# Performance work log

Hardware: AMD Instinct MI355X
Metric: run time of the kernel (lower is better)

## Reference

```python
import jax, jax.numpy as jnp
import numpy as np

N_FEAT = 512
K = 4
H = 128
N_PAIRS = N_FEAT * (N_FEAT - 1) // 2  # 130816

# Upper-triangle pair indices in the same (j1, j2>j1) row-major order as the loops
_I1, _I2 = np.triu_indices(N_FEAT, k=1)
_I1 = jnp.asarray(_I1)
_I2 = jnp.asarray(_I2)


def setup_inputs() -> dict:
    key = jax.random.key(0)
    ks = jax.random.split(key, 8)
    B = 512
    x = jax.random.normal(ks[0], (B, N_FEAT), dtype=jnp.float32)
    fm_w = jax.random.normal(ks[1], (N_FEAT, K), dtype=jnp.float32) * 0.05
    w1 = jax.random.normal(ks[2], (N_FEAT, H), dtype=jnp.float32) * (1.0 / np.sqrt(N_FEAT))
    b1 = jnp.zeros((H,), dtype=jnp.float32)
    w2 = jax.random.normal(ks[3], (H, H), dtype=jnp.float32) * (1.0 / np.sqrt(H))
    b2 = jnp.zeros((H,), dtype=jnp.float32)
    wo = jax.random.normal(ks[4], (N_PAIRS + H, 1), dtype=jnp.float32) * 0.001
    bo = jnp.zeros((1,), dtype=jnp.float32)
    return {"x": x, "fm_w": fm_w, "w1": w1, "b1": b1, "w2": w2, "b2": b2, "wo": wo, "bo": bo}


def reference(x, fm_w, w1, b1, w2, b2, wo, bo):
    # FM pairwise interactions: <w_j1, w_j2> * x[:, j1] * x[:, j2] for j1 < j2.
    # The original unrolls O(B * n^2) tiny 1xK matmuls; algebraically this is a
    # gather of the Gram matrix S = W W^T at the upper-triangle pairs.
    S = fm_w @ fm_w.T                      # [n, n], tiny (512x512)
    pair_dot = S[_I1, _I2]                 # [n_pairs]
    fm = x[:, _I1] * x[:, _I2] * pair_dot  # [B, n_pairs] -- dominant memory traffic

    # Deep part: two relu Dense layers
    h1 = jax.nn.relu(x @ w1 + b1)          # [B, 128]
    h2 = jax.nn.relu(h1 @ w2 + b2)         # [B, 128]

    feat = jnp.concatenate([fm, h2], axis=1)  # [B, n_pairs + 128]
    out = jax.nn.sigmoid(feat @ wo + bo)       # [B, 1]
    return out
```

## Files before the change

### kernel.cpp

```cpp
#include <hip/hip_runtime.h>
#include <math.h>

#define NF 512
#define HD 128
#define NB 512
#define NPAIRS 130816

#define WS_ACC 262144

__device__ __forceinline__ int xswz(int j, int h) {
  int a = (j << 5) + (h << 4);
  a ^= (j & 0x60);
  a ^= ((j & 0x80) >> 3);
  return a >> 2;
}

__global__ __launch_bounds__(256) void k_build(
    const float* __restrict__ fmw, const float* __restrict__ wo,
    float* __restrict__ ws) {
  if (blockIdx.x == 1024) {
    int t = threadIdx.x;
    ws[WS_ACC + t] = 0.f;
    ws[WS_ACC + 256 + t] = 0.f;
    return;
  }
  int t = blockIdx.x * 256 + threadIdx.x;
  int j1 = t >> 9, j2 = t & 511;
  const float4* fw = (const float4*)fmw;
  float4 a = fw[j1], b = fw[j2];
  float dot = a.x * b.x + a.y * b.y + a.z * b.z + a.w * b.w;
  float m = 0.f;
  if (j2 > j1) {
    int idx = j1 * (1023 - j1) / 2 + (j2 - j1 - 1);
    m = dot * wo[idx];
  }
  ws[t] = m;
}

__global__ __launch_bounds__(256, 2) void k_fm(
    const float* __restrict__ x, float* __restrict__ ws) {
  __shared__ float xt[4096];
  __shared__ float red[4][8];
  const int tid = threadIdx.x;
  const int bg = blockIdx.x >> 3;
  const int jc = blockIdx.x & 7;
  const int b0 = bg * 8;

  #pragma unroll
  for (int half = 0; half < 2; ++half) {
    int j = tid + half * 256;
    float xr[8];
    #pragma unroll
    for (int r = 0; r < 8; ++r) xr[r] = x[(b0 + r) * NF + j];
    *(float4*)&xt[xswz(j, 0)] = make_float4(xr[0], xr[1], xr[2], xr[3]);
    *(float4*)&xt[xswz(j, 1)] = make_float4(xr[4], xr[5], xr[6], xr[7]);
  }
  __syncthreads();

  const int j1g = tid & 7;
  const int j2s = tid >> 3;
  const int j1base = jc * 64 + j1g * 8;
  const int j2base = j2s * 16;

  float tmp[8][8];
  #pragma unroll
  for (int i = 0; i < 8; ++i)
    #pragma unroll
    for (int r = 0; r < 8; ++r) tmp[i][r] = 0.f;

  #pragma unroll
  for (int c = 0; c < 4; ++c) {
    float xv[4][8];
    #pragma unroll
    for (int e = 0; e < 4; ++e) {
      int j2 = j2base + c * 4 + e;
      float4 lo = *(const float4*)&xt[xswz(j2, 0)];
      float4 hi = *(const float4*)&xt[xswz(j2, 1)];
      xv[e][0] = lo.x; xv[e][1] = lo.y; xv[e][2] = lo.z; xv[e][3] = lo.w;
      xv[e][4] = hi.x; xv[e][5] = hi.y; xv[e][6] = hi.z; xv[e][7] = hi.w;
    }
    #pragma unroll
    for (int i = 0; i < 8; ++i) {
      const float4 m4 = *(const float4*)&ws[(j1base + i) * NF + j2base + c * 4];
      float mm[4] = {m4.x, m4.y, m4.z, m4.w};
      #pragma unroll
      for (int e = 0; e < 4; ++e)
        #pragma unroll
        for (int r = 0; r < 8; ++r)
          tmp[i][r] += mm[e] * xv[e][r];
    }
  }

  float acc[8];
  #pragma unroll
  for (int r = 0; r < 8; ++r) acc[r] = 0.f;
  #pragma unroll
  for (int i = 0; i < 8; ++i) {
    int j1 = j1base + i;
    float4 lo = *(const float4*)&xt[xswz(j1, 0)];
    float4 hi = *(const float4*)&xt[xswz(j1, 1)];
    float xj[8] = {lo.x, lo.y, lo.z, lo.w, hi.x, hi.y, hi.z, hi.w};
    #pragma unroll
    for (int r = 0; r < 8; ++r) acc[r] += tmp[i][r] * xj[r];
  }

  #pragma unroll
  for (int off = 32; off > 0; off >>= 1)
    #pragma unroll
    for (int r = 0; r < 8; ++r) acc[r] += __shfl_down(acc[r], off, 64);
  const int wave = tid >> 6, lane = tid & 63;
  if (lane == 0)
    #pragma unroll
    for (int r = 0; r < 8; ++r) red[wave][r] = acc[r];
  __syncthreads();
  if (tid < 8) {
    float s = red[0][tid] + red[1][tid] + red[2][tid] + red[3][tid];
    atomicAdd(&ws[WS_ACC + b0 + tid], s);
  }
}

__global__ __launch_bounds__(256) void k_deep(
    const float* __restrict__ x, const float* __restrict__ w1,
    const float* __restrict__ b1, const float* __restrict__ w2,
    const float* __restrict__ b2v, const float* __restrict__ wo,
    const float* __restrict__ bo, const float* __restrict__ ws,
    float* __restrict__ out) {
  __shared__ float xs[2][512];
  __shared__ float p1[2][2][128];
  __shared__ float h1[2][128];
  __shared__ float p2[2][2][128];
  __shared__ float wpart[4];
  const int tid = threadIdx.x;
  const int b0 = blockIdx.x * 2;
  const int h = tid & 127, jh = tid >> 7;

  #pragma unroll
  for (int r = 0; r < 2; ++r) {
    xs[r][tid] = x[(b0 + r) * NF + tid];
    xs[r][tid + 256] = x[(b0 + r) * NF + tid + 256];
  }
  __syncthreads();

  float a0 = 0.f, a1 = 0.f;
  const float* w1p = w1 + h;
  for (int j = 0; j < 256; ++j) {
    int jj = jh * 256 + j;
    float w = w1p[jj * 128];
    a0 += xs[0][jj] * w;
    a1 += xs[1][jj] * w;
  }
  p1[jh][0][h] = a0;
  p1[jh][1][h] = a1;
  __syncthreads();
  {
    int r = jh;
    float v = p1[0][r][h] + p1[1][r][h] + b1[h];
    h1[r][h] = v > 0.f ? v : 0.f;
  }
  __syncthreads();

  float c0 = 0.f, c1 = 0.f;
  const float* w2p = w2 + h;
  for (int k = 0; k < 64; ++k) {
    int kk = jh * 64 + k;
    float w = w2p[kk * 128];
    c0 += h1[0][kk] * w;
    c1 += h1[1][kk] * w;
  }
  p2[jh][0][h] = c0;
  p2[jh][1][h] = c1;
  __syncthreads();

  float val;
  {
    int r = jh;
    float v = p2[0][r][h] + p2[1][r][h] + b2v[h];
    v = v > 0.f ? v : 0.f;
    val = v * wo[NPAIRS + h];
  }
  #pragma unroll
  for (int off = 32; off > 0; off >>= 1) val += __shfl_down(val, off, 64);
  const int wave = tid >> 6, lane = tid & 63;
  if (lane == 0) wpart[wave] = val;
  __syncthreads();
  if (tid < 2) {
    float z = wpart[tid * 2] + wpart[tid * 2 + 1] + bo[0] + ws[WS_ACC + b0 + tid];
    out[b0 + tid] = 1.f / (1.f + expf(-z));
  }
}

extern "C" void kernel_launch(void* const* d_in, const int* in_sizes, int n_in,
                              void* d_out, int out_size, void* d_ws, size_t ws_size,
                              hipStream_t stream) {
  const float* x   = (const float*)d_in[0];
  const float* fmw = (const float*)d_in[1];
  const float* w1  = (const float*)d_in[2];
  const float* b1  = (const float*)d_in[3];
  const float* w2  = (const float*)d_in[4];
  const float* b2  = (const float*)d_in[5];
  const float* wo  = (const float*)d_in[6];
  const float* bo  = (const float*)d_in[7];
  float* out = (float*)d_out;
  float* ws  = (float*)d_ws;

  hipLaunchKernelGGL(k_build, dim3(1025), dim3(256), 0, stream, fmw, wo, ws);
  hipLaunchKernelGGL(k_fm,    dim3(512),  dim3(256), 0, stream, x, ws);
  hipLaunchKernelGGL(k_deep,  dim3(256),  dim3(256), 0, stream, x, w1, b1, w2, b2,
                     wo, bo, ws, out);
}
```

Baseline: 96.06 us.

## Repartition FM kernel, drop atomics, pre-transpose deep weights for vector loads

The FM kernel now splits the j1 range into 32 chunks across 2048 blocks. Each wave reads x and the pair-weight matrix directly from global memory with float4 loads, with no LDS staging. Per-chunk partial sums go to separate workspace slots instead of an atomicAdd accumulator, and the deep kernel reduces them. The build kernel also transposes w1 and w2 into the workspace so the deep kernel, now 512 threads, can read contiguous float4 rows. The aim is more parallelism and fewer strided loads, at the cost of extra transposes and more global-memory traffic in the FM kernel.

After: 93.35 us. 2.8% less time.

```diff
diff --git a/kernel.cpp b/kernel.cpp
--- a/kernel.cpp
+++ b/kernel.cpp
@@ -7,185 +7,171 @@
 #define NPAIRS 130816
 
 #define WS_ACC 262144
-
-__device__ __forceinline__ int xswz(int j, int h) {
-  int a = (j << 5) + (h << 4);
-  a ^= (j & 0x60);
-  a ^= ((j & 0x80) >> 3);
-  return a >> 2;
-}
+#define WS_W1T 278528
+#define WS_W2T 344064
 
 __global__ __launch_bounds__(256) void k_build(
     const float* __restrict__ fmw, const float* __restrict__ wo,
+    const float* __restrict__ w1, const float* __restrict__ w2,
     float* __restrict__ ws) {
-  if (blockIdx.x == 1024) {
-    int t = threadIdx.x;
-    ws[WS_ACC + t] = 0.f;
-    ws[WS_ACC + 256 + t] = 0.f;
-    return;
+  const int bid = blockIdx.x;
+  if (bid < 1024) {
+    int t = bid * 256 + threadIdx.x;
+    int j1 = t >> 9, j2 = t & 511;
+    const float4* fw = (const float4*)fmw;
+    float4 a = fw[j1], b = fw[j2];
+    float dot = a.x * b.x + a.y * b.y + a.z * b.z + a.w * b.w;
+    float m = 0.f;
+    if (j2 > j1) {
+      int idx = j1 * (1023 - j1) / 2 + (j2 - j1 - 1);
+      m = dot * wo[idx];
+    }
+    ws[t] = m;
+  } else if (bid < 1152) {
+    int e = (bid - 1024) * 512 + threadIdx.x;
+#pragma unroll
+    for (int u = 0; u < 2; ++u, e += 256) {
+      int k = e >> 7, h = e & 127;
+      ws[WS_W1T + h * 512 + k] = w1[e];
+    }
+  } else {
+    int e = (bid - 1152) * 512 + threadIdx.x;
+#pragma unroll
+    for (int u = 0; u < 2; ++u, e += 256) {
+      int k = e >> 7, h = e & 127;
+      ws[WS_W2T + h * 128 + k] = w2[e];
+    }
   }
-  int t = blockIdx.x * 256 + threadIdx.x;
-  int j1 = t >> 9, j2 = t & 511;
-  const float4* fw = (const float4*)fmw;
-  float4 a = fw[j1], b = fw[j2];
-  float dot = a.x * b.x + a.y * b.y + a.z * b.z + a.w * b.w;
-  float m = 0.f;
-  if (j2 > j1) {
-    int idx = j1 * (1023 - j1) / 2 + (j2 - j1 - 1);
-    m = dot * wo[idx];
-  }
-  ws[t] = m;
 }
 
-__global__ __launch_bounds__(256, 2) void k_fm(
+__global__ __launch_bounds__(256) void k_fm(
     const float* __restrict__ x, float* __restrict__ ws) {
-  __shared__ float xt[4096];
+  const int tid = threadIdx.x;
+  const int bg = blockIdx.x >> 5;
+  const int jc = blockIdx.x & 31;
+  const int b0 = bg * 8;
+  const int lane = tid & 63;
+  const int wv = tid >> 6;
+  const int j1base = jc * 16 + wv * 4;
+  const float4* x4 = (const float4*)x;
+  const float4* m4 = (const float4*)ws;
+
+  float tmp[4][8];
+#pragma unroll
+  for (int i = 0; i < 4; ++i)
+#pragma unroll
+    for (int r = 0; r < 8; ++r) tmp[i][r] = 0.f;
+
+#pragma unroll
+  for (int it = 0; it < 2; ++it) {
+    const int j2q = lane + it * 64;
+    float4 xq[8];
+#pragma unroll
+    for (int r = 0; r < 8; ++r) xq[r] = x4[(b0 + r) * 128 + j2q];
+    float4 mm[4];
+#pragma unroll
+    for (int i = 0; i < 4; ++i) mm[i] = m4[(j1base + i) * 128 + j2q];
+#pragma unroll
+    for (int i = 0; i < 4; ++i)
+#pragma unroll
+      for (int r = 0; r < 8; ++r)
+        tmp[i][r] += mm[i].x * xq[r].x + mm[i].y * xq[r].y +
+                     mm[i].z * xq[r].z + mm[i].w * xq[r].w;
+  }
+
+  float acc[8];
+#pragma unroll
+  for (int r = 0; r < 8; ++r) acc[r] = 0.f;
+#pragma unroll
+  for (int i = 0; i < 4; ++i)
+#pragma unroll
+    for (int r = 0; r < 8; ++r)
+      acc[r] += tmp[i][r] * x[(b0 + r) * NF + j1base + i];
+
+#pragma unroll
+  for (int off = 32; off > 0; off >>= 1)
+#pragma unroll
+    for (int r = 0; r < 8; ++r) acc[r] += __shfl_down(acc[r], off, 64);
+
   __shared__ float red[4][8];
+  if (lane == 0)
+#pragma unroll
+    for (int r = 0; r < 8; ++r) red[wv][r] = acc[r];
+  __syncthreads();
+  if (tid < 8)
+    ws[WS_ACC + jc * 512 + b0 + tid] =
+        red[0][tid] + red[1][tid] + red[2][tid] + red[3][tid];
+}
+
+__global__ __launch_bounds__(512) void k_deep(
+    const float* __restrict__ x, const float* __restrict__ b1,
+    const float* __restrict__ b2, const float* __restrict__ wo,
+    const float* __restrict__ bo, const float* __restrict__ ws,
+    float* __restrict__ out) {
+  __shared__ float xs[1024];
+  __shared__ float p1[4][2][128];
+  __shared__ float h1[2][128];
+  __shared__ float p2[4][2][128];
+  __shared__ float prod[2][128];
   const int tid = threadIdx.x;
-  const int bg = blockIdx.x >> 3;
-  const int jc = blockIdx.x & 7;
-  const int b0 = bg * 8;
+  const int b0 = blockIdx.x * 2;
 
-  #pragma unroll
-  for (int half = 0; half < 2; ++half) {
-    int j = tid + half * 256;
-    float xr[8];
-    #pragma unroll
-    for (int r = 0; r < 8; ++r) xr[r] = x[(b0 + r) * NF + j];
-    *(float4*)&xt[xswz(j, 0)] = make_float4(xr[0], xr[1], xr[2], xr[3]);
-    *(float4*)&xt[xswz(j, 1)] = make_float4(xr[4], xr[5], xr[6], xr[7]);
+  xs[tid] = x[b0 * NF + tid];
+  xs[tid + 512] = x[b0 * NF + 512 + tid];
+  __syncthreads();
+
+  const int h = tid & 127, part = tid >> 7;
+  const float4* w1t4 = (const float4*)(ws + WS_W1T);
+  const float4* xs4 = (const float4*)xs;
+
+  float a0 = 0.f, a1 = 0.f;
+#pragma unroll
+  for (int q = 0; q < 32; ++q) {
+    float4 w = w1t4[h * 128 + part * 32 + q];
+    float4 v0 = xs4[part * 32 + q];
+    float4 v1 = xs4[128 + part * 32 + q];
+    a0 += w.x * v0.x + w.y * v0.y + w.z * v0.z + w.w * v0.w;
+    a1 += w.x * v1.x + w.y * v1.y + w.z * v1.z + w.w * v1.w;
+  }
+  p1[part][0][h] = a0;
+  p1[part][1][h] = a1;
+  __syncthreads();
+  if (tid < 256) {
+    int r = tid >> 7, hh = tid & 127;
+    float v = p1[0][r][hh] + p1[1][r][hh] + p1[2][r][hh] + p1[3][r][hh] + b1[hh];
+    h1[r][hh] = fmaxf(v, 0.f);
   }
   __syncthreads();
 
-  const int j1g = tid & 7;
-  const int j2s = tid >> 3;
-  const int j1base = jc * 64 + j1g * 8;
-  const int j2base = j2s * 16;
-
-  float tmp[8][8];
-  #pragma unroll
-  for (int i = 0; i < 8; ++i)
-    #pragma unroll
-    for (int r = 0; r < 8; ++r) tmp[i][r] = 0.f;
-
-  #pragma unroll
-  for (int c = 0; c < 4; ++c) {
-    float xv[4][8];
-    #pragma unroll
-    for (int e = 0; e < 4; ++e) {
-      int j2 = j2base + c * 4 + e;
-      float4 lo = *(const float4*)&xt[xswz(j2, 0)];
-      float4 hi = *(const float4*)&xt[xswz(j2, 1)];
-      xv[e][0] = lo.x; xv[e][1] = lo.y; xv[e][2] = lo.z; xv[e][3] = lo.w;
-      xv[e][4] = hi.x; xv[e][5] = hi.y; xv[e][6] = hi.z; xv[e][7] = hi.w;
-    }
-    #pragma unroll
-    for (int i = 0; i < 8; ++i) {
-      const float4 m4 = *(const float4*)&ws[(j1base + i) * NF + j2base + c * 4];
-      float mm[4] = {m4.x, m4.y, m4.z, m4.w};
-      #pragma unroll
-      for (int e = 0; e < 4; ++e)
-        #pragma unroll
-        for (int r = 0; r < 8; ++r)
-          tmp[i][r] += mm[e] * xv[e][r];
-    }
+  const float4* w2t4 = (const float4*)(ws + WS_W2T);
+  const float4* h14 = (const float4*)h1;
+  float c0 = 0.f, c1 = 0.f;
+#pragma unroll
+  for (int q = 0; q < 8; ++q) {
+    float4 w = w2t4[h * 32 + part * 8 + q];
+    float4 y0 = h14[part * 8 + q];
+    float4 y1 = h14[32 + part * 8 + q];
+    c0 += w.x * y0.x + w.y * y0.y + w.z * y0.z + w.w * y0.w;
+    c1 += w.x * y1.x + w.y * y1.y + w.z * y1.z + w.w * y1.w;
   }
-
-  float acc[8];
-  #pragma unroll
-  for (int r = 0; r < 8; ++r) acc[r] = 0.f;
-  #pragma unroll
-  for (int i = 0; i < 8; ++i) {
-    int j1 = j1base + i;
-    float4 lo = *(const float4*)&xt[xswz(j1, 0)];
-    float4 hi = *(const float4*)&xt[xswz(j1, 1)];
-    float xj[8] = {lo.x, lo.y, lo.z, lo.w, hi.x, hi.y, hi.z, hi.w};
-    #pragma unroll
-    for (int r = 0; r < 8; ++r) acc[r] += tmp[i][r] * xj[r];
-  }
-
-  #pragma unroll
-  for (int off = 32; off > 0; off >>= 1)
-    #pragma unroll
-    for (int r = 0; r < 8; ++r) acc[r] += __shfl_down(acc[r], off, 64);
-  const int wave = tid >> 6, lane = tid & 63;
-  if (lane == 0)
-    #pragma unroll
-    for (int r = 0; r < 8; ++r) red[wave][r] = acc[r];
+  p2[part][0][h] = c0;
+  p2[part][1][h] = c1;
   __syncthreads();
-  if (tid < 8) {
-    float s = red[0][tid] + red[1][tid] + red[2][tid] + red[3][tid];
-    atomicAdd(&ws[WS_ACC + b0 + tid], s);
-  }
-}
-
-__global__ __launch_bounds__(256) void k_deep(
-    const float* __restrict__ x, const float* __restrict__ w1,
-    const float* __restrict__ b1, const float* __restrict__ w2,
-    const float* __restrict__ b2v, const float* __restrict__ wo,
-    const float* __restrict__ bo, const float* __restrict__ ws,
-    float* __restrict__ out) {
-  __shared__ float xs[2][512];
-  __shared__ float p1[2][2][128];
-  __shared__ float h1[2][128];
-  __shared__ float p2[2][2][128];
-  __shared__ float wpart[4];
-  const int tid = threadIdx.x;
-  const int b0 = blockIdx.x * 2;
-  const int h = tid & 127, jh = tid >> 7;
-
-  #pragma unroll
-  for (int r = 0; r < 2; ++r) {
-    xs[r][tid] = x[(b0 + r) * NF + tid];
-    xs[r][tid + 256] = x[(b0 + r) * NF + tid + 256];
+  if (tid < 256) {
+    int r = tid >> 7, hh = tid & 127;
+    float v = p2[0][r][hh] + p2[1][r][hh] + p2[2][r][hh] + p2[3][r][hh] + b2[hh];
+    v = fmaxf(v, 0.f);
+    prod[r][hh] = v * wo[NPAIRS + hh];
   }
   __syncthreads();
 
-  float a0 = 0.f, a1 = 0.f;
-  const float* w1p = w1 + h;
-  for (int j = 0; j < 256; ++j) {
-    int jj = jh * 256 + j;
-    float w = w1p[jj * 128];
-    a0 += xs[0][jj] * w;
-    a1 += xs[1][jj] * w;
-  }
-  p1[jh][0][h] = a0;
-  p1[jh][1][h] = a1;
-  __syncthreads();
-  {
-    int r = jh;
-    float v = p1[0][r][h] + p1[1][r][h] + b1[h];
-    h1[r][h] = v > 0.f ? v : 0.f;
-  }
-  __syncthreads();
-
-  float c0 = 0.f, c1 = 0.f;
-  const float* w2p = w2 + h;
-  for (int k = 0; k < 64; ++k) {
-    int kk = jh * 64 + k;
-    float w = w2p[kk * 128];
-    c0 += h1[0][kk] * w;
-    c1 += h1[1][kk] * w;
-  }
-  p2[jh][0][h] = c0;
-  p2[jh][1][h] = c1;
-  __syncthreads();
-
-  float val;
-  {
-    int r = jh;
-    float v = p2[0][r][h] + p2[1][r][h] + b2v[h];
-    v = v > 0.f ? v : 0.f;
-    val = v * wo[NPAIRS + h];
-  }
-  #pragma unroll
-  for (int off = 32; off > 0; off >>= 1) val += __shfl_down(val, off, 64);
-  const int wave = tid >> 6, lane = tid & 63;
-  if (lane == 0) wpart[wave] = val;
-  __syncthreads();
-  if (tid < 2) {
-    float z = wpart[tid * 2] + wpart[tid * 2 + 1] + bo[0] + ws[WS_ACC + b0 + tid];
-    out[b0 + tid] = 1.f / (1.f + expf(-z));
+  if (tid < 128) {
+    int r = tid >> 6, lane = tid & 63;
+    float s = prod[r][lane] + prod[r][lane + 64];
+    if (lane < 32) s += ws[WS_ACC + lane * 512 + b0 + r];
+#pragma unroll
+    for (int off = 32; off > 0; off >>= 1) s += __shfl_down(s, off, 64);
+    if (lane == 0) out[b0 + r] = 1.f / (1.f + expf(-(s + bo[0])));
   }
 }
 
@@ -203,8 +189,8 @@
   float* out = (float*)d_out;
   float* ws  = (float*)d_ws;
 
-  hipLaunchKernelGGL(k_build, dim3(1025), dim3(256), 0, stream, fmw, wo, ws);
-  hipLaunchKernelGGL(k_fm,    dim3(512),  dim3(256), 0, stream, x, ws);
-  hipLaunchKernelGGL(k_deep,  dim3(256),  dim3(256), 0, stream, x, w1, b1, w2, b2,
-                     wo, bo, ws, out);
+  hipLaunchKernelGGL(k_build, dim3(1184), dim3(256), 0, stream, fmw, wo, w1, w2, ws);
+  hipLaunchKernelGGL(k_fm,    dim3(2048), dim3(256), 0, stream, x, ws);
+  hipLaunchKernelGGL(k_deep,  dim3(256),  dim3(512), 0, stream, x, b1, b2, wo, bo,
+                     ws, out);
 }
```
